# Kernel tuning notes

Measured on AMD Instinct MI355X. Metric: run time of the kernel, lower is better.

The kernel has to match this reference:

```python
import jax, jax.numpy as jnp
import numpy as np

HEAD_DIM = 32
N_HEADS = 8
Q_DIM = 128
FF_DIM = 4 * Q_DIM
EPS = 1e-5


def layernorm(x, gamma, beta):
    mu = jnp.mean(x, axis=-1, keepdims=True)
    var = jnp.var(x, axis=-1, keepdims=True)
    return (x - mu) * jax.lax.rsqrt(var + EPS) * gamma + beta


def setup_inputs() -> dict:
    key = jax.random.key(0)
    ks = jax.random.split(key, 20)
    S, B = 1024, 16
    sc_in = 1.0 / np.sqrt(Q_DIM)
    sc_hd = 1.0 / np.sqrt(N_HEADS * HEAD_DIM)
    sc_ff = 1.0 / np.sqrt(FF_DIM)
    return {
        "sequence": jax.random.normal(ks[0], (S, B, Q_DIM), jnp.float32),
        # per-head Q/K/V projections, stacked over heads: [H, Q_dim, head_dim]
        "Wq": jax.random.uniform(ks[1], (N_HEADS, Q_DIM, HEAD_DIM), jnp.float32, -sc_in, sc_in),
        "bq": jax.random.uniform(ks[2], (N_HEADS, HEAD_DIM), jnp.float32, -sc_in, sc_in),
        "Wk": jax.random.uniform(ks[3], (N_HEADS, Q_DIM, HEAD_DIM), jnp.float32, -sc_in, sc_in),
        "bk": jax.random.uniform(ks[4], (N_HEADS, HEAD_DIM), jnp.float32, -sc_in, sc_in),
        "Wv": jax.random.uniform(ks[5], (N_HEADS, Q_DIM, HEAD_DIM), jnp.float32, -sc_in, sc_in),
        "bv": jax.random.uniform(ks[6], (N_HEADS, HEAD_DIM), jnp.float32, -sc_in, sc_in),
        # post_head_linear: [H*head_dim, Q_dim]
        "Wo": jax.random.uniform(ks[7], (N_HEADS * HEAD_DIM, Q_DIM), jnp.float32, -sc_hd, sc_hd),
        "bo": jax.random.uniform(ks[8], (Q_DIM,), jnp.float32, -sc_hd, sc_hd),
        # norm1 (note: original reuses norm1 for both layernorms)
        "gamma1": jnp.ones((Q_DIM,), jnp.float32),
        "beta1": jnp.zeros((Q_DIM,), jnp.float32),
        # FFN: Q_dim -> 4Q -> 4Q -> Q_dim
        "W1": jax.random.uniform(ks[9], (Q_DIM, FF_DIM), jnp.float32, -sc_in, sc_in),
        "b1": jax.random.uniform(ks[10], (FF_DIM,), jnp.float32, -sc_in, sc_in),
        "W2": jax.random.uniform(ks[11], (FF_DIM, FF_DIM), jnp.float32, -sc_ff, sc_ff),
        "b2": jax.random.uniform(ks[12], (FF_DIM,), jnp.float32, -sc_ff, sc_ff),
        "W3": jax.random.uniform(ks[13], (FF_DIM, Q_DIM), jnp.float32, -sc_ff, sc_ff),
        "b3": jax.random.uniform(ks[14], (Q_DIM,), jnp.float32, -sc_ff, sc_ff),
    }


def reference(sequence, Wq, bq, Wk, bk, Wv, bv, Wo, bo, gamma1, beta1, W1, b1, W2, b2, W3, b3):
    # sequence: [S, B, Q_dim] -> batch-first [B, S, Q_dim]
    x = jnp.transpose(sequence, (1, 0, 2))
    # batched per-head projections: [B, H, S, d]
    q = jnp.einsum('bsq,hqd->bhsd', x, Wq) + bq[None, :, None, :]
    k = jnp.einsum('bsq,hqd->bhsd', x, Wk) + bk[None, :, None, :]
    v = jnp.einsum('bsq,hqd->bhsd', x, Wv) + bv[None, :, None, :]
    scores = jnp.einsum('bhsd,bhtd->bhst', q, k) / np.sqrt(HEAD_DIM)
    attn = jax.nn.softmax(scores, axis=-1)
    o = jnp.einsum('bhst,bhtd->bhsd', attn, v)  # [B, H, S, d]
    B, H, S, d = o.shape
    o = jnp.transpose(o, (0, 2, 1, 3)).reshape(B, S, H * d)  # concat heads
    att_outs = o @ Wo + bo
    att_outs = layernorm(x + att_outs, gamma1, beta1)
    h = jax.nn.relu(att_outs @ W1 + b1)
    h = jax.nn.relu(h @ W2 + b2)
    h = h @ W3 + b3
    out = layernorm(att_outs + h, gamma1, beta1)  # original reuses norm1
    return jnp.transpose(out, (1, 0, 2))  # back to [S, B, Q_dim]
```

## Files before the change

kernel.cpp:

```cpp
#include <hip/hip_runtime.h>
#include <hip/hip_bf16.h>

#define S_LEN 1024
#define BATCH 16
#define QD 128
#define NH 8
#define HD 32
#define FF 512
#define NROWS (BATCH * S_LEN)
#define EPS 1e-5f

typedef __attribute__((ext_vector_type(4))) float f32x4;
typedef __attribute__((ext_vector_type(8))) short s16x8;
typedef __attribute__((ext_vector_type(4))) short s16x4;

__device__ __forceinline__ ushort f2bfu(float f) {
    union { float f; unsigned u; } v; v.f = f;
    unsigned r = (v.u + 0x7FFFu + ((v.u >> 16) & 1u)) >> 16;
    return (ushort)r;
}

__device__ __forceinline__ float bf2f(ushort u) {
    union { unsigned u; float f; } v; v.u = ((unsigned)u) << 16;
    return v.f;
}

__device__ __forceinline__ float exp2_fast(float x) {
#if __has_builtin(__builtin_amdgcn_exp2f)
    return __builtin_amdgcn_exp2f(x);
#else
    float r;
    asm("v_exp_f32 %0, %1" : "=v"(r) : "v"(x));
    return r;
#endif
}

__device__ __forceinline__ unsigned pk_bf16(float a, float b) {
    union { __hip_bfloat162 h; unsigned u; } c;
    c.h = __float22bfloat162_rn(make_float2(a, b));
    return c.u;
}

static __device__ __forceinline__ f32x4 mfma16(s16x4 a, s16x4 b, f32x4 c) {
#if __has_builtin(__builtin_amdgcn_mfma_f32_16x16x16bf16_1k)
    return __builtin_amdgcn_mfma_f32_16x16x16bf16_1k(a, b, c, 0, 0, 0);
#else
    asm volatile("v_mfma_f32_16x16x16_bf16 %0, %1, %2, %0" : "+v"(c) : "v"(a), "v"(b));
    return c;
#endif
}

static __device__ __forceinline__ f32x4 mfma32(s16x8 a, s16x8 b, f32x4 c) {
    return __builtin_amdgcn_mfma_f32_16x16x32_bf16(a, b, c, 0, 0, 0);
}

__device__ __forceinline__ void gl_lds16(const void* g, void* l) {
    __builtin_amdgcn_global_load_lds(
        (const __attribute__((address_space(1))) void*)g,
        (__attribute__((address_space(3))) void*)l, 16, 0, 0);
}

template <int K>
__device__ __forceinline__ void gemm_core(
    const ushort* __restrict__ act, const ushort* __restrict__ WTp,
    char* lds, int tok0, f32x4 acc[8]) {
    const int tid = threadIdx.x;
    const int w = tid >> 6, lane = tid & 63;
    const int qi = lane & 15, g = lane >> 4;
    const int r8 = tid >> 3;
    const int csw = (tid & 7) ^ (r8 & 7);
    const int wave_base = w * 1024;
    constexpr int NT = K / 64;

    auto STAGE = [&](int b, int ks) {
        char* buf = lds + b * 24576;
#pragma unroll
        for (int i = 0; i < 4; ++i)
            gl_lds16(WTp + (size_t)(i * 32 + r8) * K + ks + csw * 8,
                     buf + i * 4096 + wave_base);
#pragma unroll
        for (int j = 0; j < 2; ++j)
            gl_lds16(act + (size_t)(tok0 + j * 32 + r8) * K + ks + csw * 8,
                     buf + 16384 + j * 4096 + wave_base);
    };

    STAGE(0, 0);
    int cur = 0;
#pragma unroll 1
    for (int t = 0; t < NT; ++t) {
        if (t < NT - 1) {
            STAGE(cur ^ 1, (t + 1) * 64);
            asm volatile("s_waitcnt vmcnt(6)" ::: "memory");
        } else {
            asm volatile("s_waitcnt vmcnt(0)" ::: "memory");
        }
        __builtin_amdgcn_sched_barrier(0);
        __builtin_amdgcn_s_barrier();
        __builtin_amdgcn_sched_barrier(0);
        const char* A = lds + cur * 24576;
        const char* B = A + 16384;
        const int brow = w * 16 + qi;
        __builtin_amdgcn_s_setprio(1);
#pragma unroll
        for (int kk2 = 0; kk2 < 2; ++kk2) {
            s16x8 bfrag = *(const s16x8*)(B + brow * 128 +
                                          (((kk2 * 4 + g) ^ (brow & 7)) * 16));
#pragma unroll
            for (int f = 0; f < 8; ++f) {
                const int row = qi + 16 * f;
                s16x8 afrag = *(const s16x8*)(A + row * 128 +
                                              (((kk2 * 4 + g) ^ (row & 7)) * 16));
                acc[f] = mfma32(afrag, bfrag, acc[f]);
            }
        }
        __builtin_amdgcn_s_setprio(0);
        __builtin_amdgcn_sched_barrier(0);
        __builtin_amdgcn_s_barrier();
        __builtin_amdgcn_sched_barrier(0);
        cur ^= 1;
    }
}

__global__ __launch_bounds__(256) void prep_all(
    const float* __restrict__ seq, ushort* __restrict__ x_bf,
    const float* __restrict__ Wo, const float* __restrict__ W1,
    const float* __restrict__ W2, const float* __restrict__ W3,
    const float* __restrict__ Wq, const float* __restrict__ Wk,
    const float* __restrict__ Wv,
    ushort* __restrict__ WoT, ushort* __restrict__ W1T,
    ushort* __restrict__ W2T, ushort* __restrict__ W3T,
    ushort* __restrict__ WqkvT) {
    if (blockIdx.x < 2048) {
        int t = blockIdx.x * 256 + threadIdx.x;
        int e4 = t * 4;
        int s = e4 >> 11, b = (e4 >> 7) & 15, c = e4 & 127;
        float4 v = *(const float4*)(seq + e4);
        ushort4 o = {f2bfu(v.x), f2bfu(v.y), f2bfu(v.z), f2bfu(v.w)};
        *(ushort4*)(x_bf + ((size_t)(b * 1024 + s)) * 128 + c) = o;
        return;
    }
    int idx = (blockIdx.x - 2048) * 256 + threadIdx.x;
    if (idx < 32768) {
        int n = idx >> 8, k = idx & 255;
        WoT[n * 256 + k] = f2bfu(Wo[k * 128 + n]);
    } else if (idx < 98304) {
        int i = idx - 32768; int n = i >> 7, k = i & 127;
        W1T[n * 128 + k] = f2bfu(W1[k * 512 + n]);
    } else if (idx < 360448) {
        int i = idx - 98304; int n = i >> 9, k = i & 511;
        W2T[n * 512 + k] = f2bfu(W2[k * 512 + n]);
    } else if (idx < 425984) {
        int i = idx - 360448; int n = i >> 9, k = i & 511;
        W3T[n * 512 + k] = f2bfu(W3[k * 128 + n]);
    } else {
        int i = idx - 425984;
        int n = i >> 7, k = i & 127;
        int p = n >> 8, h = (n >> 5) & 7, d = n & 31;
        const float* W = (p == 0) ? Wq : (p == 1) ? Wk : Wv;
        WqkvT[n * 128 + k] = f2bfu(W[(h * QD + k) * HD + d]);
    }
}

__global__ __launch_bounds__(256) void qkv_mfma(
    const ushort* __restrict__ x_bf, const ushort* __restrict__ WqkvT,
    const float* __restrict__ bq, const float* __restrict__ bk,
    const float* __restrict__ bv,
    ushort* __restrict__ q_bf, ushort* __restrict__ k_bf,
    ushort* __restrict__ vT) {
    __shared__ __align__(16) char lds[2 * 24576];
    const int lane = threadIdx.x & 63;
    const int w = threadIdx.x >> 6;
    const int qi = lane & 15, g = lane >> 4;
    const int tok0 = blockIdx.x * 64;
    const int tok = tok0 + w * 16 + qi;
    const int n0 = blockIdx.y * 128;

    f32x4 acc[8];
#pragma unroll
    for (int f = 0; f < 8; ++f) acc[f] = (f32x4){0.f, 0.f, 0.f, 0.f};
    gemm_core<128>(x_bf, WqkvT + (size_t)n0 * 128, lds, tok0, acc);

    const int b = tok >> 10, s = tok & 1023;
    const float SCALE = 0.25503491f;
    if (n0 < 256) {
#pragma unroll
        for (int f = 0; f < 8; ++f)
#pragma unroll
            for (int r = 0; r < 4; ++r) {
                int n = n0 + 16 * f + 4 * g + r;
                int h = (n >> 5) & 7, d = n & 31;
                q_bf[((size_t)(b * 8 + h) * 1024 + s) * 32 + d] =
                    f2bfu((acc[f][r] + bq[h * 32 + d]) * SCALE);
            }
    } else if (n0 < 512) {
#pragma unroll
        for (int f = 0; f < 8; ++f)
#pragma unroll
            for (int r = 0; r < 4; ++r) {
                int n = n0 + 16 * f + 4 * g + r;
                int h = (n >> 5) & 7, d = n & 31;
                k_bf[((size_t)(b * 8 + h) * 1024 + s) * 32 + d] =
                    f2bfu(acc[f][r] + bk[h * 32 + d]);
            }
    } else {
#pragma unroll
        for (int f = 0; f < 8; ++f)
#pragma unroll
            for (int r = 0; r < 4; ++r) {
                int n = n0 + 16 * f + 4 * g + r;
                int h = (n >> 5) & 7, d = n & 31;
                vT[((size_t)(b * 8 + h) * 32 + d) * 1024 + s] =
                    f2bfu(acc[f][r] + bv[h * 32 + d]);
            }
    }
}

__global__ __launch_bounds__(512) void attn_mfma(
    const ushort* __restrict__ qb, const ushort* __restrict__ kb,
    const ushort* __restrict__ vtb, ushort* __restrict__ o_bf) {
    __shared__ __align__(16) char lds[2][8192];
    const int tid = threadIdx.x;
    const int w = tid >> 6, lane = tid & 63;
    const int g = lane >> 4, qi = lane & 15;
    const int bid = blockIdx.x;
    const int swz = (bid & 7) * 128 + (bid >> 3);
    const int bh = swz >> 3;
    const int qtile = (swz & 7) * 8 + w;

    const ushort* Kb = kb + (size_t)bh * S_LEN * HD;
    const ushort* VTb = vtb + (size_t)bh * HD * S_LEN;
    const s16x8 qf = *(const s16x8*)(qb + ((size_t)bh * S_LEN + qtile * 16 + qi) * HD + g * 8);

    const int krow = 16 * w + (lane >> 2);
    const int ksrc = (lane & 3) ^ ((lane >> 3) & 3);
    const int wv = w & 3;
    const int vrow = 8 * wv + (lane >> 3);
    const int vsrc = (lane & 7) ^ ((4 * wv + (lane >> 4)) & 7);

#define STAGE(bufp, k0)                                                        \
    do {                                                                       \
        if (w < 4)                                                             \
            gl_lds16(Kb + (size_t)((k0) + krow) * HD + ksrc * 8,               \
                     (bufp) + w * 1024);                                       \
        else                                                                   \
            gl_lds16(VTb + (size_t)vrow * S_LEN + (k0) + vsrc * 8,             \
                     (bufp) + 4096 + wv * 1024);                               \
    } while (0)

    f32x4 ot0 = {0.f, 0.f, 0.f, 0.f};
    f32x4 ot1 = {0.f, 0.f, 0.f, 0.f};
    float m_run = -1e30f, l_run = 0.f;
    const f32x4 zero = {0.f, 0.f, 0.f, 0.f};

    const int koff = (g ^ ((qi >> 1) & 3)) * 16;
    const int vs = (qi >> 1) & 7;

    STAGE(lds[0], 0);
    int cur = 0;
#pragma unroll 1
    for (int t = 0; t < 16; ++t) {
        if (t < 15) {
            STAGE(lds[cur ^ 1], (t + 1) * 64);
            asm volatile("s_waitcnt vmcnt(1)" ::: "memory");
        } else {
            asm volatile("s_waitcnt vmcnt(0)" ::: "memory");
        }
        __builtin_amdgcn_sched_barrier(0);
        __builtin_amdgcn_s_barrier();
        __builtin_amdgcn_sched_barrier(0);

        const char* kl = lds[cur];
        const char* vl = lds[cur] + 4096;
        s16x8 ka[4];
#pragma unroll
        for (int kt = 0; kt < 4; ++kt)
            ka[kt] = *(const s16x8*)(kl + (16 * kt + qi) * 64 + koff);
        s16x4 va[2][4];
#pragma unroll
        for (int h = 0; h < 2; ++h)
#pragma unroll
            for (int kt = 0; kt < 4; ++kt) {
                int c8 = 4 * kt + g;
                va[h][kt] = *(const s16x4*)(vl + (16 * h + qi) * 128 +
                                            (((c8 >> 1) ^ vs) * 16) + (c8 & 1) * 8);
            }

        f32x4 st[4];
        __builtin_amdgcn_s_setprio(1);
#pragma unroll
        for (int kt = 0; kt < 4; ++kt) st[kt] = mfma32(ka[kt], qf, zero);
        __builtin_amdgcn_s_setprio(0);

        float a0 = fmaxf(fmaxf(st[0][0], st[0][1]), fmaxf(st[0][2], st[0][3]));
        float a1 = fmaxf(fmaxf(st[1][0], st[1][1]), fmaxf(st[1][2], st[1][3]));
        float a2 = fmaxf(fmaxf(st[2][0], st[2][1]), fmaxf(st[2][2], st[2][3]));
        float a3 = fmaxf(fmaxf(st[3][0], st[3][1]), fmaxf(st[3][2], st[3][3]));
        float pmax = fmaxf(fmaxf(a0, a1), fmaxf(a2, a3));

        if (!__all(pmax <= m_run + 8.0f)) {
            float mt = pmax;
            mt = fmaxf(mt, __shfl_xor(mt, 16, 64));
            mt = fmaxf(mt, __shfl_xor(mt, 32, 64));
            float m_new = fmaxf(m_run, mt);
            float alpha = exp2_fast(m_run - m_new);
            l_run *= alpha;
#pragma unroll
            for (int r = 0; r < 4; ++r) { ot0[r] *= alpha; ot1[r] *= alpha; }
            m_run = m_new;
        }

        float p[4][4];
#pragma unroll
        for (int kt = 0; kt < 4; ++kt)
#pragma unroll
            for (int r = 0; r < 4; ++r) p[kt][r] = exp2_fast(st[kt][r] - m_run);
        float s0 = (p[0][0] + p[0][1]) + (p[0][2] + p[0][3]);
        float s1 = (p[1][0] + p[1][1]) + (p[1][2] + p[1][3]);
        float s2 = (p[2][0] + p[2][1]) + (p[2][2] + p[2][3]);
        float s3 = (p[3][0] + p[3][1]) + (p[3][2] + p[3][3]);
        l_run += (s0 + s1) + (s2 + s3);

        union { s16x4 v; uint2 u; } pb[4];
#pragma unroll
        for (int kt = 0; kt < 4; ++kt) {
            pb[kt].u.x = pk_bf16(p[kt][0], p[kt][1]);
            pb[kt].u.y = pk_bf16(p[kt][2], p[kt][3]);
        }
        __builtin_amdgcn_s_setprio(1);
#pragma unroll
        for (int kt = 0; kt < 4; ++kt) {
            ot0 = mfma16(va[0][kt], pb[kt].v, ot0);
            ot1 = mfma16(va[1][kt], pb[kt].v, ot1);
        }
        __builtin_amdgcn_s_setprio(0);

        __builtin_amdgcn_sched_barrier(0);
        __builtin_amdgcn_s_barrier();
        __builtin_amdgcn_sched_barrier(0);
        cur ^= 1;
    }
#undef STAGE

    l_run += __shfl_xor(l_run, 16, 64);
    l_run += __shfl_xor(l_run, 32, 64);
    const float inv_l = 1.0f / l_run;
    const int b = bh >> 3, head = bh & 7;
    const int qg = qtile * 16 + qi;
    ushort* orow = o_bf + ((size_t)(b * S_LEN + qg)) * (NH * HD) + head * HD;
    ushort4 ob0 = {f2bfu(ot0[0] * inv_l), f2bfu(ot0[1] * inv_l),
                   f2bfu(ot0[2] * inv_l), f2bfu(ot0[3] * inv_l)};
    ushort4 ob1 = {f2bfu(ot1[0] * inv_l), f2bfu(ot1[1] * inv_l),
                   f2bfu(ot1[2] * inv_l), f2bfu(ot1[3] * inv_l)};
    *(ushort4*)(orow + g * 4) = ob0;
    *(ushort4*)(orow + 16 + g * 4) = ob1;
}

__global__ __launch_bounds__(256) void wo_ln_mfma(
    const ushort* __restrict__ o_bf, const ushort* __restrict__ WoT,
    const float* __restrict__ bo, const float* __restrict__ seq,
    const float* __restrict__ gamma, const float* __restrict__ beta,
    ushort* __restrict__ att_bf) {
    __shared__ __align__(16) char lds[2 * 24576];
    const int lane = threadIdx.x & 63;
    const int w = threadIdx.x >> 6;
    const int qi = lane & 15, g = lane >> 4;
    const int tok0 = blockIdx.x * 64;
    const int tok = tok0 + w * 16 + qi;

    f32x4 acc[8];
#pragma unroll
    for (int f = 0; f < 8; ++f) acc[f] = (f32x4){0.f, 0.f, 0.f, 0.f};
    gemm_core<256>(o_bf, WoT, lds, tok0, acc);

    const int b = tok >> 10, s = tok & 1023;
    const float* xrow = seq + (size_t)(s * BATCH + b) * QD;
    float sum = 0.f, sumsq = 0.f;
#pragma unroll
    for (int f = 0; f < 8; ++f) {
        const int c = 16 * f + 4 * g;
        float4 bv = *(const float4*)(bo + c);
        float4 xv = *(const float4*)(xrow + c);
        acc[f][0] += bv.x + xv.x;
        acc[f][1] += bv.y + xv.y;
        acc[f][2] += bv.z + xv.z;
        acc[f][3] += bv.w + xv.w;
#pragma unroll
        for (int r = 0; r < 4; ++r) { sum += acc[f][r]; sumsq += acc[f][r] * acc[f][r]; }
    }
    sum += __shfl_xor(sum, 16, 64);
    sum += __shfl_xor(sum, 32, 64);
    sumsq += __shfl_xor(sumsq, 16, 64);
    sumsq += __shfl_xor(sumsq, 32, 64);
    const float mu = sum * (1.0f / QD);
    const float var = sumsq * (1.0f / QD) - mu * mu;
    const float rstd = rsqrtf(var + EPS);

#pragma unroll
    for (int f = 0; f < 8; ++f) {
        const int c = 16 * f + 4 * g;
        float4 gm = *(const float4*)(gamma + c);
        float4 bt = *(const float4*)(beta + c);
        ushort4 pv;
        pv.x = f2bfu((acc[f][0] - mu) * rstd * gm.x + bt.x);
        pv.y = f2bfu((acc[f][1] - mu) * rstd * gm.y + bt.y);
        pv.z = f2bfu((acc[f][2] - mu) * rstd * gm.z + bt.z);
        pv.w = f2bfu((acc[f][3] - mu) * rstd * gm.w + bt.w);
        *(ushort4*)(att_bf + (size_t)tok * QD + c) = pv;
    }
}

template <int K>
__global__ __launch_bounds__(256) void ffn_mfma(
    const ushort* __restrict__ act, const ushort* __restrict__ WT,
    const float* __restrict__ bias, ushort* __restrict__ out, int N) {
    __shared__ __align__(16) char lds[2 * 24576];
    const int lane = threadIdx.x & 63;
    const int w = threadIdx.x >> 6;
    const int qi = lane & 15, g = lane >> 4;
    const int tok0 = blockIdx.x * 64;
    const int tok = tok0 + w * 16 + qi;
    const int n0 = blockIdx.y * 128;

    f32x4 acc[8];
#pragma unroll
    for (int f = 0; f < 8; ++f) acc[f] = (f32x4){0.f, 0.f, 0.f, 0.f};
    gemm_core<K>(act, WT + (size_t)n0 * K, lds, tok0, acc);

#pragma unroll
    for (int f = 0; f < 8; ++f) {
        const int c = n0 + 16 * f + 4 * g;
        float4 bv = *(const float4*)(bias + c);
        ushort4 pv;
        pv.x = f2bfu(fmaxf(acc[f][0] + bv.x, 0.f));
        pv.y = f2bfu(fmaxf(acc[f][1] + bv.y, 0.f));
        pv.z = f2bfu(fmaxf(acc[f][2] + bv.z, 0.f));
        pv.w = f2bfu(fmaxf(acc[f][3] + bv.w, 0.f));
        *(ushort4*)(out + (size_t)tok * N + c) = pv;
    }
}

__global__ __launch_bounds__(256) void w3_ln_mfma(
    const ushort* __restrict__ h2, const ushort* __restrict__ W3T,
    const float* __restrict__ b3, const ushort* __restrict__ att_bf,
    const float* __restrict__ gamma, const float* __restrict__ beta,
    float* __restrict__ out) {
    __shared__ __align__(16) char lds[2 * 24576];
    const int lane = threadIdx.x & 63;
    const int w = threadIdx.x >> 6;
    const int qi = lane & 15, g = lane >> 4;
    const int tok0 = blockIdx.x * 64;
    const int tok = tok0 + w * 16 + qi;

    f32x4 acc[8];
#pragma unroll
    for (int f = 0; f < 8; ++f) acc[f] = (f32x4){0.f, 0.f, 0.f, 0.f};
    gemm_core<512>(h2, W3T, lds, tok0, acc);

    float sum = 0.f, sumsq = 0.f;
#pragma unroll
    for (int f = 0; f < 8; ++f) {
        const int c = 16 * f + 4 * g;
        float4 bv = *(const float4*)(b3 + c);
        ushort4 xv = *(const ushort4*)(att_bf + (size_t)tok * QD + c);
        acc[f][0] += bv.x + bf2f(xv.x);
        acc[f][1] += bv.y + bf2f(xv.y);
        acc[f][2] += bv.z + bf2f(xv.z);
        acc[f][3] += bv.w + bf2f(xv.w);
#pragma unroll
        for (int r = 0; r < 4; ++r) { sum += acc[f][r]; sumsq += acc[f][r] * acc[f][r]; }
    }
    sum += __shfl_xor(sum, 16, 64);
    sum += __shfl_xor(sum, 32, 64);
    sumsq += __shfl_xor(sumsq, 16, 64);
    sumsq += __shfl_xor(sumsq, 32, 64);
    const float mu = sum * (1.0f / QD);
    const float var = sumsq * (1.0f / QD) - mu * mu;
    const float rstd = rsqrtf(var + EPS);

    const int b = tok >> 10, s = tok & 1023;
    float* orow = out + (size_t)(s * BATCH + b) * QD;
#pragma unroll
    for (int f = 0; f < 8; ++f) {
        const int c = 16 * f + 4 * g;
        float4 gm = *(const float4*)(gamma + c);
        float4 bt = *(const float4*)(beta + c);
        float4 ov;
        ov.x = (acc[f][0] - mu) * rstd * gm.x + bt.x;
        ov.y = (acc[f][1] - mu) * rstd * gm.y + bt.y;
        ov.z = (acc[f][2] - mu) * rstd * gm.z + bt.z;
        ov.w = (acc[f][3] - mu) * rstd * gm.w + bt.w;
        *(float4*)(orow + c) = ov;
    }
}

extern "C" void kernel_launch(void* const* d_in, const int* in_sizes, int n_in,
                              void* d_out, int out_size, void* d_ws, size_t ws_size,
                              hipStream_t stream) {
    const float* seq = (const float*)d_in[0];
    const float* Wq = (const float*)d_in[1];
    const float* bq = (const float*)d_in[2];
    const float* Wk = (const float*)d_in[3];
    const float* bk = (const float*)d_in[4];
    const float* Wv = (const float*)d_in[5];
    const float* bv = (const float*)d_in[6];
    const float* Wo = (const float*)d_in[7];
    const float* bo = (const float*)d_in[8];
    const float* gamma = (const float*)d_in[9];
    const float* beta = (const float*)d_in[10];
    const float* W1 = (const float*)d_in[11];
    const float* b1 = (const float*)d_in[12];
    const float* W2 = (const float*)d_in[13];
    const float* b2 = (const float*)d_in[14];
    const float* W3 = (const float*)d_in[15];
    const float* b3 = (const float*)d_in[16];

    char* wsb = (char*)d_ws;
    ushort* q_bf  = (ushort*)(wsb);
    ushort* k_bf  = (ushort*)(wsb + (8ull << 20));
    ushort* vT    = (ushort*)(wsb + (16ull << 20));
    ushort* o_bf  = (ushort*)(wsb + (24ull << 20));
    ushort* att_bf= (ushort*)(wsb + (40ull << 20));
    ushort* h1_bf = (ushort*)(wsb);
    ushort* h2_bf = (ushort*)(wsb + (16ull << 20));
    ushort* x_bf  = (ushort*)(wsb + (45ull << 20));
    ushort* WoT   = (ushort*)(wsb + (49ull << 20));
    ushort* W1T   = WoT + 32768;
    ushort* W2T   = W1T + 65536;
    ushort* W3T   = W2T + 262144;
    ushort* WqkvT = W3T + 65536;
    float* out = (float*)d_out;

    prep_all<<<4096, 256, 0, stream>>>(seq, x_bf, Wo, W1, W2, W3, Wq, Wk, Wv,
                                       WoT, W1T, W2T, W3T, WqkvT);
    qkv_mfma<<<dim3(NROWS / 64, 6), 256, 0, stream>>>(x_bf, WqkvT, bq, bk, bv,
                                                      q_bf, k_bf, vT);
    attn_mfma<<<1024, 512, 0, stream>>>(q_bf, k_bf, vT, o_bf);
    wo_ln_mfma<<<NROWS / 64, 256, 0, stream>>>(o_bf, WoT, bo, seq, gamma, beta, att_bf);
    ffn_mfma<QD><<<dim3(NROWS / 64, 4), 256, 0, stream>>>(att_bf, W1T, b1, h1_bf, FF);
    ffn_mfma<FF><<<dim3(NROWS / 64, 4), 256, 0, stream>>>(h1_bf, W2T, b2, h2_bf, FF);
    w3_ln_mfma<<<NROWS / 64, 256, 0, stream>>>(h2_bf, W3T, b3, att_bf, gamma, beta, out);
}
```

Measured before the change: 109.2 us.

## Deepen attention K/V prefetch to four LDS buffers and vectorize Q/K stores

The attention kernel moves from double buffering to a four-slot LDS ring with three tiles in flight. The prefetch is issued after the top-of-loop barrier, which lets the trailing barrier be removed so each iteration syncs only once. Separately, the QKV projection epilogue now writes Q and K as packed 4-element bf16 vectors instead of scalar stores. LDS use per attention block doubles to 32KB, which could reduce occupancy, and the buffer-reuse safety now depends on the single-barrier ordering.

```diff
diff --git a/kernel.cpp b/kernel.cpp
--- a/kernel.cpp
+++ b/kernel.cpp
@@ -184,24 +184,26 @@
     const float SCALE = 0.25503491f;
     if (n0 < 256) {
 #pragma unroll
-        for (int f = 0; f < 8; ++f)
-#pragma unroll
-            for (int r = 0; r < 4; ++r) {
-                int n = n0 + 16 * f + 4 * g + r;
-                int h = (n >> 5) & 7, d = n & 31;
-                q_bf[((size_t)(b * 8 + h) * 1024 + s) * 32 + d] =
-                    f2bfu((acc[f][r] + bq[h * 32 + d]) * SCALE);
-            }
+        for (int f = 0; f < 8; ++f) {
+            int n = n0 + 16 * f + 4 * g;
+            int h = (n >> 5) & 7, d = n & 31;
+            ushort4 pv = {f2bfu((acc[f][0] + bq[h * 32 + d + 0]) * SCALE),
+                          f2bfu((acc[f][1] + bq[h * 32 + d + 1]) * SCALE),
+                          f2bfu((acc[f][2] + bq[h * 32 + d + 2]) * SCALE),
+                          f2bfu((acc[f][3] + bq[h * 32 + d + 3]) * SCALE)};
+            *(ushort4*)(q_bf + ((size_t)(b * 8 + h) * 1024 + s) * 32 + d) = pv;
+        }
     } else if (n0 < 512) {
 #pragma unroll
-        for (int f = 0; f < 8; ++f)
-#pragma unroll
-            for (int r = 0; r < 4; ++r) {
-                int n = n0 + 16 * f + 4 * g + r;
-                int h = (n >> 5) & 7, d = n & 31;
-                k_bf[((size_t)(b * 8 + h) * 1024 + s) * 32 + d] =
-                    f2bfu(acc[f][r] + bk[h * 32 + d]);
-            }
+        for (int f = 0; f < 8; ++f) {
+            int n = n0 + 16 * f + 4 * g;
+            int h = (n >> 5) & 7, d = n & 31;
+            ushort4 pv = {f2bfu(acc[f][0] + bk[h * 32 + d + 0]),
+                          f2bfu(acc[f][1] + bk[h * 32 + d + 1]),
+                          f2bfu(acc[f][2] + bk[h * 32 + d + 2]),
+                          f2bfu(acc[f][3] + bk[h * 32 + d + 3])};
+            *(ushort4*)(k_bf + ((size_t)(b * 8 + h) * 1024 + s) * 32 + d) = pv;
+        }
     } else {
 #pragma unroll
         for (int f = 0; f < 8; ++f)
@@ -218,7 +220,7 @@
 __global__ __launch_bounds__(512) void attn_mfma(
     const ushort* __restrict__ qb, const ushort* __restrict__ kb,
     const ushort* __restrict__ vtb, ushort* __restrict__ o_bf) {
-    __shared__ __align__(16) char lds[2][8192];
+    __shared__ __align__(16) char lds[4][8192];
     const int tid = threadIdx.x;
     const int w = tid >> 6, lane = tid & 63;
     const int g = lane >> 4, qi = lane & 15;
@@ -256,21 +258,23 @@
     const int vs = (qi >> 1) & 7;
 
     STAGE(lds[0], 0);
-    int cur = 0;
+    STAGE(lds[1], 64);
+    STAGE(lds[2], 128);
 #pragma unroll 1
     for (int t = 0; t < 16; ++t) {
-        if (t < 15) {
-            STAGE(lds[cur ^ 1], (t + 1) * 64);
+        if (t <= 13)
+            asm volatile("s_waitcnt vmcnt(2)" ::: "memory");
+        else if (t == 14)
             asm volatile("s_waitcnt vmcnt(1)" ::: "memory");
-        } else {
+        else
             asm volatile("s_waitcnt vmcnt(0)" ::: "memory");
-        }
         __builtin_amdgcn_sched_barrier(0);
         __builtin_amdgcn_s_barrier();
         __builtin_amdgcn_sched_barrier(0);
-
-        const char* kl = lds[cur];
-        const char* vl = lds[cur] + 4096;
+        if (t <= 12) STAGE(lds[(t + 3) & 3], (t + 3) * 64);
+
+        const char* kl = lds[t & 3];
+        const char* vl = kl + 4096;
         s16x8 ka[4];
 #pragma unroll
         for (int kt = 0; kt < 4; ++kt)
@@ -333,11 +337,6 @@
             ot1 = mfma16(va[1][kt], pb[kt].v, ot1);
         }
         __builtin_amdgcn_s_setprio(0);
-
-        __builtin_amdgcn_sched_barrier(0);
-        __builtin_amdgcn_s_barrier();
-        __builtin_amdgcn_sched_barrier(0);
-        cur ^= 1;
     }
 #undef STAGE
 
```

After: 109.1 us. No clear change (-0.1%).
